# Kernel tuning notes

Hardware: AMD Instinct MI355X
Metric: run time of the kernel (lower is better)

Reference implementation:

```python
import jax, jax.numpy as jnp
import numpy as np

C = 256
C8 = C // 8
B, D, H, W = 2, 16, 64, 64


def setup_inputs() -> dict:
    key = jax.random.key(0)
    ks = jax.random.split(key, 8)
    s = 0.05
    return {
        "x1": jax.random.normal(ks[0], (B, C, D, H, W), dtype=jnp.float32),
        "x2": jax.random.normal(ks[1], (B, C, D, H, W), dtype=jnp.float32),
        "Wq": jax.random.normal(ks[2], (C8, C), dtype=jnp.float32) * s,
        "bq": jax.random.normal(ks[3], (C8,), dtype=jnp.float32) * s,
        "Wk": jax.random.normal(ks[4], (C8, C), dtype=jnp.float32) * s,
        "bk": jax.random.normal(ks[5], (C8,), dtype=jnp.float32) * s,
        "Wv": jax.random.normal(ks[6], (C, C), dtype=jnp.float32) * s,
        "bv": jax.random.normal(ks[7], (C,), dtype=jnp.float32) * s,
    }


def _conv1x1(x, Wt, b):
    # 1x1x1 Conv3d == channel-mixing linear: x [B,Cin,D,H,W], Wt [Cout,Cin]
    return jnp.einsum('bcdhw,oc->bodhw', x, Wt) + b[None, :, None, None, None]


def reference(x1, x2, Wq, bq, Wk, bk, Wv, bv):
    q = _conv1x1(x1, Wq, bq)   # [B,C8,D,H,W]
    k = _conv1x1(x2, Wk, bk)   # [B,C8,D,H,W]
    v = _conv1x1(x2, Wv, bv)   # [B,C, D,H,W]
    # Non-softmax bilinear attention over the W axis, batched over (b,d,h)
    attn = jnp.einsum('bcdhx,bcdhy->bdhxy', q, k)        # [B,D,H,W,W]
    out = jnp.einsum('bdhxy,bcdhy->bcdhx', attn, v)      # [B,C,D,H,W]
    return out
```

## Files before the change

### kernel.cpp

```cpp
#include <hip/hip_runtime.h>

#define NB   2
#define ND   16
#define NH   64
#define DHW  65536
#define HW   4096
#define CDHW 16777216

typedef __attribute__((ext_vector_type(4))) float f32x4;
typedef __attribute__((ext_vector_type(8))) short bf16x8;
typedef unsigned short ushort_t;

#define MFMA16(a, b, c) __builtin_amdgcn_mfma_f32_16x16x32_bf16((a), (b), (c), 0, 0, 0)

#define OFF_XTH 0
#define OFF_XTL 8192
#define OFF_AH  0
#define OFF_AL  8192
#define OFF_R2  16384
#define OFF_QH  32768
#define OFF_QL  36864
#define OFF_KH  40960
#define OFF_KL  45056
#define SMEM_BYTES 49152

#define WS_WQH 0
#define WS_WQL 8192
#define WS_WKH 16384
#define WS_WKL 24576
#define WS_WVH 32768
#define WS_WVL 98304
#define WS_W_BYTES ((size_t)163840 * 2)

__device__ __forceinline__ void split_val(float f, short& h, short& l) {
  unsigned int u = __builtin_bit_cast(unsigned int, f);
  h = (short)(unsigned short)(u >> 16);
  float fh = __builtin_bit_cast(float, u & 0xffff0000u);
  float r = f - fh;
  l = (short)(unsigned short)(__builtin_bit_cast(unsigned int, r) >> 16);
}

__device__ __forceinline__ void load_split8(const float* __restrict__ p, bf16x8& h8, bf16x8& l8) {
  float4 a = *(const float4*)p;
  float4 b = *(const float4*)(p + 4);
  float f[8] = {a.x, a.y, a.z, a.w, b.x, b.y, b.z, b.w};
#pragma unroll
  for (int j = 0; j < 8; ++j) {
    short hh, ll;
    split_val(f[j], hh, ll);
    h8[j] = hh; l8[j] = ll;
  }
}

__device__ __forceinline__ int swzb(int row, int colb) {
  return row * 128 + (((colb) & ~15) ^ ((row & 7) << 4)) + ((colb) & 15);
}

__global__ void prep_w(const float* __restrict__ Wq, const float* __restrict__ Wk,
                       const float* __restrict__ Wv, ushort_t* __restrict__ ws) {
  int idx = blockIdx.x * 256 + threadIdx.x;
  const float* src; int off; ushort_t *H, *L;
  if (idx < 8192)       { src = Wq; off = idx;         H = ws + WS_WQH; L = ws + WS_WQL; }
  else if (idx < 16384) { src = Wk; off = idx - 8192;  H = ws + WS_WKH; L = ws + WS_WKL; }
  else if (idx < 81920) { src = Wv; off = idx - 16384; H = ws + WS_WVH; L = ws + WS_WVL; }
  else return;
  short h, l;
  split_val(src[off], h, l);
  H[off] = (ushort_t)h;
  L[off] = (ushort_t)l;
}

template<bool PW>
__global__ __launch_bounds__(256, 3) void xattn_fused(
    const float* __restrict__ x1, const float* __restrict__ x2,
    const float* __restrict__ Wq, const float* __restrict__ bq,
    const float* __restrict__ Wk, const float* __restrict__ bk,
    const float* __restrict__ Wv, const float* __restrict__ bv,
    const ushort_t* __restrict__ wsp, float* __restrict__ out)
{
  __shared__ char smem[SMEM_BYTES];
  char*     XthB = smem + OFF_XTH;
  char*     XtlB = smem + OFF_XTL;
  char*     AhB  = smem + OFF_AH;
  char*     AlB  = smem + OFF_AL;
  float*    Xlin = (float*)(smem + OFF_R2);
  ushort_t* Qh   = (ushort_t*)(smem + OFF_QH);
  ushort_t* Ql   = (ushort_t*)(smem + OFF_QL);
  ushort_t* Kh   = (ushort_t*)(smem + OFF_KH);
  ushort_t* Kl   = (ushort_t*)(smem + OFF_KL);

  const int tid  = threadIdx.x;
  const int lane = tid & 63;
  const int wv   = tid >> 6;
  const int l15  = lane & 15;
  const int g    = lane >> 4;

  const int bid = blockIdx.x;
  const int grp = (bid & 7) * 256 + (bid >> 3);
  const int b   = grp >> 10;
  const int rem = grp & 1023;
  const int d   = rem >> 6;
  const int h   = rem & 63;
  const size_t base = (size_t)b * CDHW + (size_t)d * HW + (size_t)h * 64;

  const ushort_t* WqH = wsp + WS_WQH;
  const ushort_t* WqL = wsp + WS_WQL;
  const ushort_t* WkH = wsp + WS_WKH;
  const ushort_t* WkL = wsp + WS_WKL;
  const ushort_t* WvH = wsp + WS_WVH;
  const ushort_t* WvL = wsp + WS_WVL;

  const float* x1p = x1 + base;
  const float* x2p = x2 + base;

  float4 pf[4];
  auto issue_pf = [&](const float* __restrict__ src) {
#pragma unroll
    for (int i = 0; i < 4; ++i) {
      int ch = 16 * wv + g + 4 * i;
      pf[i] = *(const float4*)(src + (size_t)ch * DHW + 4 * l15);
    }
  };
  auto write_xlin = [&]() {
#pragma unroll
    for (int i = 0; i < 4; ++i) {
      int ch = 16 * wv + g + 4 * i;
      *(float4*)&Xlin[ch * 64 + 4 * l15] = pf[i];
    }
  };
  auto passB = [&]() {
#pragma unroll
    for (int bb = 0; bb < 2; ++bb) {
      int c0 = 16 * wv + 8 * bb;
      bf16x8 h8, l8;
#pragma unroll
      for (int j = 0; j < 8; ++j) {
        float f = Xlin[(c0 + j) * 64 + lane];
        short hh, ll;
        split_val(f, hh, ll);
        h8[j] = hh; l8[j] = ll;
      }
      *(bf16x8*)(XthB + swzb(lane, c0 * 2)) = h8;
      *(bf16x8*)(XtlB + swzb(lane, c0 * 2)) = l8;
    }
  };
  auto ldsx = [&](const char* B, int row, int ko) -> bf16x8 {
    return *(const bf16x8*)(B + swzb(row, ko * 2));
  };

  {
    f32x4 qacc[2];
#pragma unroll
    for (int mt = 0; mt < 2; ++mt) {
      int r0 = mt * 16 + 4 * g;
      qacc[mt] = (f32x4){bq[r0], bq[r0 + 1], bq[r0 + 2], bq[r0 + 3]};
    }
    issue_pf(x1p);
    write_xlin();
    __syncthreads();
#pragma unroll
    for (int t = 0; t < 4; ++t) {
      issue_pf(t < 3 ? x1p + (size_t)(t + 1) * 64 * DHW : x2p);
      passB();
      __syncthreads();
#pragma unroll
      for (int ks = 0; ks < 2; ++ks) {
        const int ko = ks * 32 + 8 * g;
        const int kg = t * 64 + ko;
        bf16x8 bh = ldsx(XthB, 16 * wv + l15, ko);
        bf16x8 bl = ldsx(XtlB, 16 * wv + l15, ko);
#pragma unroll
        for (int mt = 0; mt < 2; ++mt) {
          bf16x8 wh, wl;
          if constexpr (PW) {
            wh = *(const bf16x8*)&WqH[(size_t)(mt * 16 + l15) * 256 + kg];
            wl = *(const bf16x8*)&WqL[(size_t)(mt * 16 + l15) * 256 + kg];
          } else {
            load_split8(Wq + (size_t)(mt * 16 + l15) * 256 + kg, wh, wl);
          }
          qacc[mt] = MFMA16(wh, bh, qacc[mt]);
          qacc[mt] = MFMA16(wh, bl, qacc[mt]);
          qacc[mt] = MFMA16(wl, bh, qacc[mt]);
        }
      }
      if (t == 3) {
        const int x = 16 * wv + l15;
#pragma unroll
        for (int mt = 0; mt < 2; ++mt)
#pragma unroll
          for (int r = 0; r < 4; ++r) {
            short hh, ll;
            split_val(qacc[mt][r], hh, ll);
            Qh[x * 32 + mt * 16 + 4 * g + r] = (ushort_t)hh;
            Ql[x * 32 + mt * 16 + 4 * g + r] = (ushort_t)ll;
          }
      }
      write_xlin();
      __syncthreads();
    }
  }

  f32x4 vacc[4][4];
  {
    f32x4 kacc[2];
#pragma unroll
    for (int mt = 0; mt < 2; ++mt) {
      int r0 = mt * 16 + 4 * g;
      kacc[mt] = (f32x4){bk[r0], bk[r0 + 1], bk[r0 + 2], bk[r0 + 3]};
    }
#pragma unroll
    for (int mt = 0; mt < 4; ++mt) {
      int r0 = 64 * wv + mt * 16 + 4 * g;
      f32x4 bb = (f32x4){bv[r0], bv[r0 + 1], bv[r0 + 2], bv[r0 + 3]};
#pragma unroll
      for (int nt = 0; nt < 4; ++nt) vacc[mt][nt] = bb;
    }
#pragma unroll
    for (int t = 0; t < 4; ++t) {
      if (t < 3) issue_pf(x2p + (size_t)(t + 1) * 64 * DHW);
      passB();
      __syncthreads();
#pragma unroll
      for (int ks = 0; ks < 2; ++ks) {
        const int ko = ks * 32 + 8 * g;
        const int kg = t * 64 + ko;
        bf16x8 xh[4], xl[4];
#pragma unroll
        for (int nt = 0; nt < 4; ++nt) {
          xh[nt] = ldsx(XthB, nt * 16 + l15, ko);
          xl[nt] = ldsx(XtlB, nt * 16 + l15, ko);
        }
        {
          bf16x8 bh = ldsx(XthB, 16 * wv + l15, ko);
          bf16x8 bl = ldsx(XtlB, 16 * wv + l15, ko);
#pragma unroll
          for (int mt = 0; mt < 2; ++mt) {
            bf16x8 wh, wl;
            if constexpr (PW) {
              wh = *(const bf16x8*)&WkH[(size_t)(mt * 16 + l15) * 256 + kg];
              wl = *(const bf16x8*)&WkL[(size_t)(mt * 16 + l15) * 256 + kg];
            } else {
              load_split8(Wk + (size_t)(mt * 16 + l15) * 256 + kg, wh, wl);
            }
            kacc[mt] = MFMA16(wh, bh, kacc[mt]);
            kacc[mt] = MFMA16(wh, bl, kacc[mt]);
            kacc[mt] = MFMA16(wl, bh, kacc[mt]);
          }
        }
        __builtin_amdgcn_s_setprio(1);
#pragma unroll
        for (int mt = 0; mt < 4; ++mt) {
          bf16x8 wh, wl;
          if constexpr (PW) {
            wh = *(const bf16x8*)&WvH[(size_t)(64 * wv + mt * 16 + l15) * 256 + kg];
            wl = *(const bf16x8*)&WvL[(size_t)(64 * wv + mt * 16 + l15) * 256 + kg];
          } else {
            load_split8(Wv + (size_t)(64 * wv + mt * 16 + l15) * 256 + kg, wh, wl);
          }
#pragma unroll
          for (int nt = 0; nt < 4; ++nt) {
            vacc[mt][nt] = MFMA16(wh, xh[nt], vacc[mt][nt]);
            vacc[mt][nt] = MFMA16(wh, xl[nt], vacc[mt][nt]);
            vacc[mt][nt] = MFMA16(wl, xh[nt], vacc[mt][nt]);
          }
        }
        __builtin_amdgcn_s_setprio(0);
      }
      if (t < 3) {
        write_xlin();
      } else {
        const int y = 16 * wv + l15;
#pragma unroll
        for (int mt = 0; mt < 2; ++mt)
#pragma unroll
          for (int r = 0; r < 4; ++r) {
            short hh, ll;
            split_val(kacc[mt][r], hh, ll);
            Kh[y * 32 + mt * 16 + 4 * g + r] = (ushort_t)hh;
            Kl[y * 32 + mt * 16 + 4 * g + r] = (ushort_t)ll;
          }
      }
      __syncthreads();
    }
  }

  {
    const int y = 16 * wv + l15;
    bf16x8 kh = *(const bf16x8*)&Kh[y * 32 + 8 * g];
    bf16x8 kl = *(const bf16x8*)&Kl[y * 32 + 8 * g];
    f32x4 acc[4];
#pragma unroll
    for (int mt = 0; mt < 4; ++mt) acc[mt] = (f32x4){0.f, 0.f, 0.f, 0.f};
#pragma unroll
    for (int mt = 0; mt < 4; ++mt) {
      bf16x8 qh = *(const bf16x8*)&Qh[(mt * 16 + l15) * 32 + 8 * g];
      bf16x8 ql = *(const bf16x8*)&Ql[(mt * 16 + l15) * 32 + 8 * g];
      acc[mt] = MFMA16(qh, kh, acc[mt]);
      acc[mt] = MFMA16(qh, kl, acc[mt]);
      acc[mt] = MFMA16(ql, kh, acc[mt]);
    }
#pragma unroll
    for (int mt = 0; mt < 4; ++mt)
#pragma unroll
      for (int r = 0; r < 4; ++r) {
        short hh, ll;
        split_val(acc[mt][r], hh, ll);
        int xr = mt * 16 + 4 * g + r;
        *(ushort_t*)(AhB + swzb(xr, y * 2)) = (ushort_t)hh;
        *(ushort_t*)(AlB + swzb(xr, y * 2)) = (ushort_t)ll;
      }
  }
  __syncthreads();

  {
    char* VhB = smem + OFF_R2 + wv * 4096;
    char* VlB = VhB + 2048;
    const int cb = 64 * wv;
#pragma unroll
    for (int mt = 0; mt < 4; ++mt) {
#pragma unroll
      for (int nt = 0; nt < 4; ++nt)
#pragma unroll
        for (int r = 0; r < 4; ++r) {
          short hh, ll;
          split_val(vacc[mt][nt][r], hh, ll);
          int colb = (nt * 16 + l15) * 2;
          *(ushort_t*)(VhB + swzb(4 * g + r, colb)) = (ushort_t)hh;
          *(ushort_t*)(VlB + swzb(4 * g + r, colb)) = (ushort_t)ll;
        }
      f32x4 oacc[4];
#pragma unroll
      for (int nt = 0; nt < 4; ++nt) oacc[nt] = (f32x4){0.f, 0.f, 0.f, 0.f};
      __builtin_amdgcn_s_setprio(1);
#pragma unroll
      for (int ys = 0; ys < 2; ++ys) {
        const int yo = ys * 32 + 8 * g;
        bf16x8 vh8 = *(const bf16x8*)(VhB + swzb(l15, yo * 2));
        bf16x8 vl8 = *(const bf16x8*)(VlB + swzb(l15, yo * 2));
#pragma unroll
        for (int nt = 0; nt < 4; ++nt) {
          bf16x8 ah8 = *(const bf16x8*)(AhB + swzb(nt * 16 + l15, yo * 2));
          bf16x8 al8 = *(const bf16x8*)(AlB + swzb(nt * 16 + l15, yo * 2));
          oacc[nt] = MFMA16(vh8, ah8, oacc[nt]);
          oacc[nt] = MFMA16(vh8, al8, oacc[nt]);
          oacc[nt] = MFMA16(vl8, ah8, oacc[nt]);
        }
      }
      __builtin_amdgcn_s_setprio(0);
#pragma unroll
      for (int nt = 0; nt < 4; ++nt)
#pragma unroll
        for (int r = 0; r < 4; ++r)
          out[base + (size_t)(cb + mt * 16 + 4 * g + r) * DHW + nt * 16 + l15] = oacc[nt][r];
    }
  }
}

extern "C" void kernel_launch(void* const* d_in, const int* in_sizes, int n_in,
                              void* d_out, int out_size, void* d_ws, size_t ws_size,
                              hipStream_t stream)
{
  const float* x1 = (const float*)d_in[0];
  const float* x2 = (const float*)d_in[1];
  const float* Wq = (const float*)d_in[2];
  const float* bq = (const float*)d_in[3];
  const float* Wk = (const float*)d_in[4];
  const float* bk = (const float*)d_in[5];
  const float* Wv = (const float*)d_in[6];
  const float* bv = (const float*)d_in[7];
  float* out = (float*)d_out;

  if (d_ws && ws_size >= WS_W_BYTES) {
    ushort_t* ws = (ushort_t*)d_ws;
    hipLaunchKernelGGL(prep_w, dim3(320), dim3(256), 0, stream, Wq, Wk, Wv, ws);
    hipLaunchKernelGGL(xattn_fused<true>, dim3(NB * ND * NH), dim3(256), 0, stream,
                       x1, x2, Wq, bq, Wk, bk, Wv, bv, ws, out);
  } else {
    hipLaunchKernelGGL(xattn_fused<false>, dim3(NB * ND * NH), dim3(256), 0, stream,
                       x1, x2, Wq, bq, Wk, bk, Wv, bv, (const ushort_t*)nullptr, out);
  }
}
```

Baseline: 226.2 us.

## Double-buffer split X tiles and use per-wave staging to cut barriers

Replaces the single shared X tile with two ping-pong bf16 hi/lo buffers and gives each wave its own fp32 staging region. The split-conversion of the next tile now overlaps the MFMA work on the current one, with one barrier per step instead of two. The Q and K/V phases are merged into one continuous pipeline over eight channel tiles. Shared memory grows to 64KB of dynamic LDS and launch bounds drop from 3 to 2 blocks per CU, trading occupancy for fewer barrier stalls.

```diff
diff --git a/kernel.cpp b/kernel.cpp
--- a/kernel.cpp
+++ b/kernel.cpp
@@ -13,16 +13,19 @@
 
 #define MFMA16(a, b, c) __builtin_amdgcn_mfma_f32_16x16x32_bf16((a), (b), (c), 0, 0, 0)
 
-#define OFF_XTH 0
-#define OFF_XTL 8192
-#define OFF_AH  0
-#define OFF_AL  8192
-#define OFF_R2  16384
-#define OFF_QH  32768
-#define OFF_QL  36864
-#define OFF_KH  40960
-#define OFF_KL  45056
-#define SMEM_BYTES 49152
+#define OFF_B0H  0
+#define OFF_B0L  8192
+#define OFF_B1H  16384
+#define OFF_B1L  24576
+#define OFF_AH   0
+#define OFF_AL   8192
+#define OFF_VB   16384
+#define OFF_WLIN 32768
+#define OFF_QH   49152
+#define OFF_QL   53248
+#define OFF_KH   57344
+#define OFF_KL   61440
+#define SMEM_BYTES 65536
 
 #define WS_WQH 0
 #define WS_WQL 8192
@@ -71,24 +74,14 @@
 }
 
 template<bool PW>
-__global__ __launch_bounds__(256, 3) void xattn_fused(
+__global__ __launch_bounds__(256, 2) void xattn_fused(
     const float* __restrict__ x1, const float* __restrict__ x2,
     const float* __restrict__ Wq, const float* __restrict__ bq,
     const float* __restrict__ Wk, const float* __restrict__ bk,
     const float* __restrict__ Wv, const float* __restrict__ bv,
     const ushort_t* __restrict__ wsp, float* __restrict__ out)
 {
-  __shared__ char smem[SMEM_BYTES];
-  char*     XthB = smem + OFF_XTH;
-  char*     XtlB = smem + OFF_XTL;
-  char*     AhB  = smem + OFF_AH;
-  char*     AlB  = smem + OFF_AL;
-  float*    Xlin = (float*)(smem + OFF_R2);
-  ushort_t* Qh   = (ushort_t*)(smem + OFF_QH);
-  ushort_t* Ql   = (ushort_t*)(smem + OFF_QL);
-  ushort_t* Kh   = (ushort_t*)(smem + OFF_KH);
-  ushort_t* Kl   = (ushort_t*)(smem + OFF_KL);
-
+  extern __shared__ char smem[];
   const int tid  = threadIdx.x;
   const int lane = tid & 63;
   const int wv   = tid >> 6;
@@ -110,8 +103,17 @@
   const ushort_t* WvH = wsp + WS_WVH;
   const ushort_t* WvL = wsp + WS_WVL;
 
+  float*    wlin = (float*)(smem + OFF_WLIN + wv * 4096);
+  ushort_t* Qh   = (ushort_t*)(smem + OFF_QH);
+  ushort_t* Ql   = (ushort_t*)(smem + OFF_QL);
+  ushort_t* Kh   = (ushort_t*)(smem + OFF_KH);
+  ushort_t* Kl   = (ushort_t*)(smem + OFF_KL);
+
   const float* x1p = x1 + base;
   const float* x2p = x2 + base;
+  auto tsrc = [&](int i) -> const float* {
+    return (i < 4) ? (x1p + (size_t)i * 64 * DHW) : (x2p + (size_t)(i - 4) * 64 * DHW);
+  };
 
   float4 pf[4];
   auto issue_pf = [&](const float* __restrict__ src) {
@@ -121,170 +123,169 @@
       pf[i] = *(const float4*)(src + (size_t)ch * DHW + 4 * l15);
     }
   };
-  auto write_xlin = [&]() {
-#pragma unroll
-    for (int i = 0; i < 4; ++i) {
-      int ch = 16 * wv + g + 4 * i;
-      *(float4*)&Xlin[ch * 64 + 4 * l15] = pf[i];
-    }
-  };
-  auto passB = [&]() {
+  auto write_wlin = [&]() {
+#pragma unroll
+    for (int i = 0; i < 4; ++i)
+      *(float4*)&wlin[(g + 4 * i) * 64 + 4 * l15] = pf[i];
+  };
+  auto passB = [&](char* th, char* tl) {
 #pragma unroll
     for (int bb = 0; bb < 2; ++bb) {
-      int c0 = 16 * wv + 8 * bb;
+      int c0 = 8 * bb;
       bf16x8 h8, l8;
 #pragma unroll
       for (int j = 0; j < 8; ++j) {
-        float f = Xlin[(c0 + j) * 64 + lane];
+        float f = wlin[(c0 + j) * 64 + lane];
         short hh, ll;
         split_val(f, hh, ll);
         h8[j] = hh; l8[j] = ll;
       }
-      *(bf16x8*)(XthB + swzb(lane, c0 * 2)) = h8;
-      *(bf16x8*)(XtlB + swzb(lane, c0 * 2)) = l8;
+      int cg = 16 * wv + c0;
+      *(bf16x8*)(th + swzb(lane, cg * 2)) = h8;
+      *(bf16x8*)(tl + swzb(lane, cg * 2)) = l8;
     }
   };
   auto ldsx = [&](const char* B, int row, int ko) -> bf16x8 {
     return *(const bf16x8*)(B + swzb(row, ko * 2));
   };
 
-  {
-    f32x4 qacc[2];
-#pragma unroll
-    for (int mt = 0; mt < 2; ++mt) {
-      int r0 = mt * 16 + 4 * g;
-      qacc[mt] = (f32x4){bq[r0], bq[r0 + 1], bq[r0 + 2], bq[r0 + 3]};
-    }
-    issue_pf(x1p);
-    write_xlin();
+  char* bufH[2] = { smem + OFF_B0H, smem + OFF_B1H };
+  char* bufL[2] = { smem + OFF_B0L, smem + OFF_B1L };
+
+  f32x4 qacc[2], kacc[2], vacc[4][4];
+#pragma unroll
+  for (int mt = 0; mt < 2; ++mt) {
+    int r0 = mt * 16 + 4 * g;
+    qacc[mt] = (f32x4){bq[r0], bq[r0 + 1], bq[r0 + 2], bq[r0 + 3]};
+    kacc[mt] = (f32x4){bk[r0], bk[r0 + 1], bk[r0 + 2], bk[r0 + 3]};
+  }
+#pragma unroll
+  for (int mt = 0; mt < 4; ++mt) {
+    int r0 = 64 * wv + mt * 16 + 4 * g;
+    f32x4 bb = (f32x4){bv[r0], bv[r0 + 1], bv[r0 + 2], bv[r0 + 3]};
+#pragma unroll
+    for (int nt = 0; nt < 4; ++nt) vacc[mt][nt] = bb;
+  }
+
+  issue_pf(tsrc(0));
+  write_wlin();
+  passB(bufH[0], bufL[0]);
+  issue_pf(tsrc(1));
+
+#pragma unroll
+  for (int t = 0; t < 4; ++t) {
     __syncthreads();
-#pragma unroll
-    for (int t = 0; t < 4; ++t) {
-      issue_pf(t < 3 ? x1p + (size_t)(t + 1) * 64 * DHW : x2p);
-      passB();
-      __syncthreads();
-#pragma unroll
-      for (int ks = 0; ks < 2; ++ks) {
-        const int ko = ks * 32 + 8 * g;
-        const int kg = t * 64 + ko;
-        bf16x8 bh = ldsx(XthB, 16 * wv + l15, ko);
-        bf16x8 bl = ldsx(XtlB, 16 * wv + l15, ko);
+    write_wlin();
+    issue_pf(tsrc(t + 2));
+    passB(bufH[(t + 1) & 1], bufL[(t + 1) & 1]);
+#pragma unroll
+    for (int ks = 0; ks < 2; ++ks) {
+      const int ko = ks * 32 + 8 * g;
+      const int kg = t * 64 + ko;
+      bf16x8 bh = ldsx(bufH[t & 1], 16 * wv + l15, ko);
+      bf16x8 bl = ldsx(bufL[t & 1], 16 * wv + l15, ko);
+#pragma unroll
+      for (int mt = 0; mt < 2; ++mt) {
+        bf16x8 wh, wl;
+        if constexpr (PW) {
+          wh = *(const bf16x8*)&WqH[(size_t)(mt * 16 + l15) * 256 + kg];
+          wl = *(const bf16x8*)&WqL[(size_t)(mt * 16 + l15) * 256 + kg];
+        } else {
+          load_split8(Wq + (size_t)(mt * 16 + l15) * 256 + kg, wh, wl);
+        }
+        qacc[mt] = MFMA16(wh, bh, qacc[mt]);
+        qacc[mt] = MFMA16(wh, bl, qacc[mt]);
+        qacc[mt] = MFMA16(wl, bh, qacc[mt]);
+      }
+    }
+    if (t == 3) {
+      const int x = 16 * wv + l15;
+#pragma unroll
+      for (int mt = 0; mt < 2; ++mt)
+#pragma unroll
+        for (int r = 0; r < 4; ++r) {
+          short hh, ll;
+          split_val(qacc[mt][r], hh, ll);
+          Qh[x * 32 + mt * 16 + 4 * g + r] = (ushort_t)hh;
+          Ql[x * 32 + mt * 16 + 4 * g + r] = (ushort_t)ll;
+        }
+    }
+  }
+
+#pragma unroll
+  for (int u = 0; u < 4; ++u) {
+    __syncthreads();
+    if (u < 3) {
+      write_wlin();
+      if (u < 2) issue_pf(tsrc(u + 6));
+      passB(bufH[(u + 1) & 1], bufL[(u + 1) & 1]);
+    }
+    const char* th = bufH[u & 1];
+    const char* tl = bufL[u & 1];
+#pragma unroll
+    for (int ks = 0; ks < 2; ++ks) {
+      const int ko = ks * 32 + 8 * g;
+      const int kg = u * 64 + ko;
+      bf16x8 xh[4], xl[4];
+#pragma unroll
+      for (int nt = 0; nt < 4; ++nt) {
+        xh[nt] = ldsx(th, nt * 16 + l15, ko);
+        xl[nt] = ldsx(tl, nt * 16 + l15, ko);
+      }
+      {
+        bf16x8 bh = ldsx(th, 16 * wv + l15, ko);
+        bf16x8 bl = ldsx(tl, 16 * wv + l15, ko);
 #pragma unroll
         for (int mt = 0; mt < 2; ++mt) {
           bf16x8 wh, wl;
           if constexpr (PW) {
-            wh = *(const bf16x8*)&WqH[(size_t)(mt * 16 + l15) * 256 + kg];
-            wl = *(const bf16x8*)&WqL[(size_t)(mt * 16 + l15) * 256 + kg];
+            wh = *(const bf16x8*)&WkH[(size_t)(mt * 16 + l15) * 256 + kg];
+            wl = *(const bf16x8*)&WkL[(size_t)(mt * 16 + l15) * 256 + kg];
           } else {
-            load_split8(Wq + (size_t)(mt * 16 + l15) * 256 + kg, wh, wl);
+            load_split8(Wk + (size_t)(mt * 16 + l15) * 256 + kg, wh, wl);
           }
-          qacc[mt] = MFMA16(wh, bh, qacc[mt]);
-          qacc[mt] = MFMA16(wh, bl, qacc[mt]);
-          qacc[mt] = MFMA16(wl, bh, qacc[mt]);
-        }
-      }
-      if (t == 3) {
-        const int x = 16 * wv + l15;
-#pragma unroll
-        for (int mt = 0; mt < 2; ++mt)
-#pragma unroll
-          for (int r = 0; r < 4; ++r) {
-            short hh, ll;
-            split_val(qacc[mt][r], hh, ll);
-            Qh[x * 32 + mt * 16 + 4 * g + r] = (ushort_t)hh;
-            Ql[x * 32 + mt * 16 + 4 * g + r] = (ushort_t)ll;
-          }
-      }
-      write_xlin();
-      __syncthreads();
-    }
-  }
-
-  f32x4 vacc[4][4];
+          kacc[mt] = MFMA16(wh, bh, kacc[mt]);
+          kacc[mt] = MFMA16(wh, bl, kacc[mt]);
+          kacc[mt] = MFMA16(wl, bh, kacc[mt]);
+        }
+      }
+      __builtin_amdgcn_s_setprio(1);
+#pragma unroll
+      for (int mt = 0; mt < 4; ++mt) {
+        bf16x8 wh, wl;
+        if constexpr (PW) {
+          wh = *(const bf16x8*)&WvH[(size_t)(64 * wv + mt * 16 + l15) * 256 + kg];
+          wl = *(const bf16x8*)&WvL[(size_t)(64 * wv + mt * 16 + l15) * 256 + kg];
+        } else {
+          load_split8(Wv + (size_t)(64 * wv + mt * 16 + l15) * 256 + kg, wh, wl);
+        }
+#pragma unroll
+        for (int nt = 0; nt < 4; ++nt) {
+          vacc[mt][nt] = MFMA16(wh, xh[nt], vacc[mt][nt]);
+          vacc[mt][nt] = MFMA16(wh, xl[nt], vacc[mt][nt]);
+          vacc[mt][nt] = MFMA16(wl, xh[nt], vacc[mt][nt]);
+        }
+      }
+      __builtin_amdgcn_s_setprio(0);
+    }
+    if (u == 3) {
+      const int y = 16 * wv + l15;
+#pragma unroll
+      for (int mt = 0; mt < 2; ++mt)
+#pragma unroll
+        for (int r = 0; r < 4; ++r) {
+          short hh, ll;
+          split_val(kacc[mt][r], hh, ll);
+          Kh[y * 32 + mt * 16 + 4 * g + r] = (ushort_t)hh;
+          Kl[y * 32 + mt * 16 + 4 * g + r] = (ushort_t)ll;
+        }
+    }
+  }
+  __syncthreads();
+
   {
-    f32x4 kacc[2];
-#pragma unroll
-    for (int mt = 0; mt < 2; ++mt) {
-      int r0 = mt * 16 + 4 * g;
-      kacc[mt] = (f32x4){bk[r0], bk[r0 + 1], bk[r0 + 2], bk[r0 + 3]};
-    }
-#pragma unroll
-    for (int mt = 0; mt < 4; ++mt) {
-      int r0 = 64 * wv + mt * 16 + 4 * g;
-      f32x4 bb = (f32x4){bv[r0], bv[r0 + 1], bv[r0 + 2], bv[r0 + 3]};
-#pragma unroll
-      for (int nt = 0; nt < 4; ++nt) vacc[mt][nt] = bb;
-    }
-#pragma unroll
-    for (int t = 0; t < 4; ++t) {
-      if (t < 3) issue_pf(x2p + (size_t)(t + 1) * 64 * DHW);
-      passB();
-      __syncthreads();
-#pragma unroll
-      for (int ks = 0; ks < 2; ++ks) {
-        const int ko = ks * 32 + 8 * g;
-        const int kg = t * 64 + ko;
-        bf16x8 xh[4], xl[4];
-#pragma unroll
-        for (int nt = 0; nt < 4; ++nt) {
-          xh[nt] = ldsx(XthB, nt * 16 + l15, ko);
-          xl[nt] = ldsx(XtlB, nt * 16 + l15, ko);
-        }
-        {
-          bf16x8 bh = ldsx(XthB, 16 * wv + l15, ko);
-          bf16x8 bl = ldsx(XtlB, 16 * wv + l15, ko);
-#pragma unroll
-          for (int mt = 0; mt < 2; ++mt) {
-            bf16x8 wh, wl;
-            if constexpr (PW) {
-              wh = *(const bf16x8*)&WkH[(size_t)(mt * 16 + l15) * 256 + kg];
-              wl = *(const bf16x8*)&WkL[(size_t)(mt * 16 + l15) * 256 + kg];
-            } else {
-              load_split8(Wk + (size_t)(mt * 16 + l15) * 256 + kg, wh, wl);
-            }
-            kacc[mt] = MFMA16(wh, bh, kacc[mt]);
-            kacc[mt] = MFMA16(wh, bl, kacc[mt]);
-            kacc[mt] = MFMA16(wl, bh, kacc[mt]);
-          }
-        }
-        __builtin_amdgcn_s_setprio(1);
-#pragma unroll
-        for (int mt = 0; mt < 4; ++mt) {
-          bf16x8 wh, wl;
-          if constexpr (PW) {
-            wh = *(const bf16x8*)&WvH[(size_t)(64 * wv + mt * 16 + l15) * 256 + kg];
-            wl = *(const bf16x8*)&WvL[(size_t)(64 * wv + mt * 16 + l15) * 256 + kg];
-          } else {
-            load_split8(Wv + (size_t)(64 * wv + mt * 16 + l15) * 256 + kg, wh, wl);
-          }
-#pragma unroll
-          for (int nt = 0; nt < 4; ++nt) {
-            vacc[mt][nt] = MFMA16(wh, xh[nt], vacc[mt][nt]);
-            vacc[mt][nt] = MFMA16(wh, xl[nt], vacc[mt][nt]);
-            vacc[mt][nt] = MFMA16(wl, xh[nt], vacc[mt][nt]);
-          }
-        }
-        __builtin_amdgcn_s_setprio(0);
-      }
-      if (t < 3) {
-        write_xlin();
-      } else {
-        const int y = 16 * wv + l15;
-#pragma unroll
-        for (int mt = 0; mt < 2; ++mt)
-#pragma unroll
-          for (int r = 0; r < 4; ++r) {
-            short hh, ll;
-            split_val(kacc[mt][r], hh, ll);
-            Kh[y * 32 + mt * 16 + 4 * g + r] = (ushort_t)hh;
-            Kl[y * 32 + mt * 16 + 4 * g + r] = (ushort_t)ll;
-          }
-      }
-      __syncthreads();
-    }
-  }
-
-  {
+    char* AhB = smem + OFF_AH;
+    char* AlB = smem + OFF_AL;
     const int y = 16 * wv + l15;
     bf16x8 kh = *(const bf16x8*)&Kh[y * 32 + 8 * g];
     bf16x8 kl = *(const bf16x8*)&Kl[y * 32 + 8 * g];
@@ -313,7 +314,9 @@
   __syncthreads();
 
   {
-    char* VhB = smem + OFF_R2 + wv * 4096;
+    const char* AhB = smem + OFF_AH;
+    const char* AlB = smem + OFF_AL;
+    char* VhB = smem + OFF_VB + wv * 4096;
     char* VlB = VhB + 2048;
     const int cb = 64 * wv;
 #pragma unroll
@@ -372,11 +375,15 @@
 
   if (d_ws && ws_size >= WS_W_BYTES) {
     ushort_t* ws = (ushort_t*)d_ws;
+    (void)hipFuncSetAttribute((const void*)xattn_fused<true>,
+                              hipFuncAttributeMaxDynamicSharedMemorySize, SMEM_BYTES);
     hipLaunchKernelGGL(prep_w, dim3(320), dim3(256), 0, stream, Wq, Wk, Wv, ws);
-    hipLaunchKernelGGL(xattn_fused<true>, dim3(NB * ND * NH), dim3(256), 0, stream,
+    hipLaunchKernelGGL(xattn_fused<true>, dim3(NB * ND * NH), dim3(256), SMEM_BYTES, stream,
                        x1, x2, Wq, bq, Wk, bk, Wv, bv, ws, out);
   } else {
-    hipLaunchKernelGGL(xattn_fused<false>, dim3(NB * ND * NH), dim3(256), 0, stream,
+    (void)hipFuncSetAttribute((const void*)xattn_fused<false>,
+                              hipFuncAttributeMaxDynamicSharedMemorySize, SMEM_BYTES);
+    hipLaunchKernelGGL(xattn_fused<false>, dim3(NB * ND * NH), dim3(256), SMEM_BYTES, stream,
                        x1, x2, Wq, bq, Wk, bk, Wv, bv, (const ushort_t*)nullptr, out);
   }
 }
```

After: 224.6 us. Within noise of the previous version (-0.7%).
